# Performance work log

Measured on AMD Instinct MI355X. Metric: run time of the kernel, lower is better.

The kernel has to match this reference:

```python
import jax, jax.numpy as jnp
import numpy as np

B, DIM, Hs, Ws = 2, 64, 48, 48
HEADS, DIM_HEAD = 4, 16
INNER = HEADS * DIM_HEAD  # 64
MLP_DIM = 256


def setup_inputs() -> dict:
    key = jax.random.key(0)
    ks = jax.random.split(key, 10)
    w = lambda k, shape: (jax.random.normal(k, shape, jnp.float32) * 0.02)
    return dict(
        x=jax.random.normal(ks[0], (B, DIM, Hs, Ws), jnp.float32),
        y=jax.random.normal(ks[1], (B, DIM, Hs, Ws), jnp.float32),
        ln1_g=jnp.ones((DIM,), jnp.float32), ln1_b=jnp.zeros((DIM,), jnp.float32),
        w_sa1=w(ks[2], (DIM, INNER)), w_sa2=w(ks[3], (DIM, INNER)),
        w_se1=w(ks[4], (DIM, INNER)), w_se2=w(ks[5], (DIM, INNER)),
        w_out=w(ks[6], (INNER, DIM)), b_out=jnp.zeros((DIM,), jnp.float32),
        ln2_g=jnp.ones((DIM,), jnp.float32), ln2_b=jnp.zeros((DIM,), jnp.float32),
        w1=w(ks[7], (DIM, MLP_DIM)), b1=jnp.zeros((MLP_DIM,), jnp.float32),
        w2=w(ks[8], (MLP_DIM, DIM)), b2=jnp.zeros((DIM,), jnp.float32),
    )


def _layer_norm(t, g, b, eps=1e-5):
    m = t.mean(-1, keepdims=True)
    v = t.var(-1, keepdims=True)
    return (t - m) * jax.lax.rsqrt(v + eps) * g + b


def reference(x, y, ln1_g, ln1_b, w_sa1, w_sa2, w_se1, w_se2, w_out, b_out,
              ln2_g, ln2_b, w1, b1, w2, b2):
    b, c, h, wdt = x.shape
    xt = x.reshape(b, c, h * wdt).transpose(0, 2, 1)  # B n C
    yt = y.reshape(b, c, h * wdt).transpose(0, 2, 1)
    n = xt.shape[1]
    scale = DIM_HEAD ** (-0.5)

    # PreNorm: same LayerNorm applied to both x and y (shared params)
    xn = _layer_norm(xt, ln1_g, ln1_b)
    yn = _layer_norm(yt, ln1_g, ln1_b)

    def split_heads(t, wm):  # B n C -> B h n d
        return (t @ wm).reshape(b, n, HEADS, DIM_HEAD).transpose(0, 2, 1, 3)

    y1 = split_heads(yn, w_sa1)
    y2 = split_heads(yn, w_sa2)
    x1 = split_heads(xn, w_se1)
    x2 = split_heads(xn, w_se2)

    # spatial attention map: n x n from y branch
    sacm = jax.nn.softmax(jnp.einsum('bhid,bhjd->bhij', y1, y2) * scale, axis=-1)
    # channel attention map: d x d from x branch
    secm = jax.nn.softmax(jnp.einsum('bhni,bhnj->bhij', x1, x2) * scale / (n / DIM_HEAD), axis=-1)

    out1 = jnp.einsum('bhij,bhjd->bhid', sacm, x1)  # spatial map applied to x values
    out2 = jnp.einsum('bhni,bhij->bhnj', y1, secm)  # channel map applied to y values
    out = (out1 * out2).transpose(0, 2, 1, 3).reshape(b, n, INNER)
    xt = xt + out @ w_out + b_out  # residual around attention

    # MLP with PreNorm + residual, LeakyReLU slope 0.01 (torch default)
    xn2 = _layer_norm(xt, ln2_g, ln2_b)
    hid = jax.nn.leaky_relu(xn2 @ w1 + b1, negative_slope=0.01)
    xt = xt + hid @ w2 + b2

    return xt.transpose(0, 2, 1).reshape(b, c, h, wdt)
```

## Files before the change

### kernel.cpp

```cpp
#include <hip/hip_runtime.h>

#define HW 2304
#define CH 64
typedef unsigned short ushort_t;
typedef __attribute__((ext_vector_type(8))) short bf16x8;
typedef __attribute__((ext_vector_type(4))) float f32x4;

#define QSCL (0.25f * 1.44269504088896340736f)
#define SECM_SCL (0.25f / 144.f)
#define MFMA(a, b, c) __builtin_amdgcn_mfma_f32_16x16x32_bf16((a), (b), (c), 0, 0, 0)

static __device__ __forceinline__ ushort_t f2bf(float f) {
    union { float f; unsigned u; } v; v.f = f;
    unsigned r = v.u + 0x7FFFu + ((v.u >> 16) & 1u);
    return (ushort_t)(r >> 16);
}
static __device__ __forceinline__ unsigned cvtpk(float a, float b) {
    unsigned r;
    asm("v_cvt_pk_bf16_f32 %0, %1, %2" : "=v"(r) : "v"(a), "v"(b));
    return r;
}
union U8 { unsigned u[4]; bf16x8 v; };

__global__ __launch_bounds__(256) void k_wconv(
    const float* __restrict__ wsa1, const float* __restrict__ wsa2,
    const float* __restrict__ wse1, const float* __restrict__ wse2,
    const float* __restrict__ w_out, const float* __restrict__ w1,
    const float* __restrict__ w2,
    ushort_t* __restrict__ wsa1T, ushort_t* __restrict__ wsa2T,
    ushort_t* __restrict__ wse1T, ushort_t* __restrict__ wse2T,
    ushort_t* __restrict__ w_outT, ushort_t* __restrict__ wT1, ushort_t* __restrict__ wT2,
    float* __restrict__ sacc)
{
    const int blk = blockIdx.x, tid = threadIdx.x;
    if (blk < 8) sacc[blk * 256 + tid] = 0.f;
    if (blk < 80) {
        const int mi = blk >> 4;
        const float* s = mi == 0 ? wsa1 : mi == 1 ? wsa2 : mi == 2 ? wse1 : mi == 3 ? wse2 : w_out;
        ushort_t* d = mi == 0 ? wsa1T : mi == 1 ? wsa2T : mi == 2 ? wse1T : mi == 3 ? wse2T : w_outT;
        const int o = (blk & 15) * 256 + tid;
        d[o] = f2bf(s[(o & 63) * 64 + (o >> 6)]);
    } else if (blk < 144) {
        const int o = (blk - 80) * 256 + tid;
        wT1[o] = f2bf(w1[(o & 63) * 256 + (o >> 6)]);
    } else {
        const int o = (blk - 144) * 256 + tid;
        wT2[o] = f2bf(w2[(o & 255) * 64 + (o >> 8)]);
    }
}

__global__ __launch_bounds__(64) void k_ln_proj(
    const float* __restrict__ x, const float* __restrict__ y,
    const float* __restrict__ g, const float* __restrict__ bb,
    const ushort_t* __restrict__ wsa1T, const ushort_t* __restrict__ wsa2T,
    const ushort_t* __restrict__ wse1T, const ushort_t* __restrict__ wse2T,
    float* __restrict__ y1f, ushort_t* __restrict__ qbf, ushort_t* __restrict__ kbf,
    ushort_t* __restrict__ vtbf, float* __restrict__ sacc)
{
    __shared__ ushort_t ldsA[16 * 24 + 32];
    __shared__ ushort_t ldsB[16 * 24 + 32];
    const int task = blockIdx.x;
    const int jt = blockIdx.y;
    const int rt = task % 144;
    const int b  = (task / 144) & 1;
    const int branch = task / 288;
    const int lane = threadIdx.x;
    const int r = lane & 15, cg = lane >> 4;
    const int q0 = rt * 16;
    const float* in = (branch ? y : x) + (size_t)b * CH * HW + q0 + r;
    float lo[8], hi[8];
    float s = 0.f, sq = 0.f;
    #pragma unroll
    for (int ki = 0; ki < 8; ++ki) {
        lo[ki] = in[(size_t)(8 * cg + ki) * HW];
        hi[ki] = in[(size_t)(32 + 8 * cg + ki) * HW];
        s += lo[ki] + hi[ki];
        sq += lo[ki] * lo[ki] + hi[ki] * hi[ki];
    }
    s  += __shfl_xor(s, 16);  s  += __shfl_xor(s, 32);
    sq += __shfl_xor(sq, 16); sq += __shfl_xor(sq, 32);
    const float m  = s * (1.f / 64.f);
    const float rs = rsqrtf(sq * (1.f / 64.f) - m * m + 1e-5f);
    float ga[16], be[16];
    {
        const float4* gp = (const float4*)g;
        const float4* bp = (const float4*)bb;
        *(float4*)&ga[0]  = gp[2 * cg];     *(float4*)&ga[4]  = gp[2 * cg + 1];
        *(float4*)&ga[8]  = gp[8 + 2 * cg]; *(float4*)&ga[12] = gp[9 + 2 * cg];
        *(float4*)&be[0]  = bp[2 * cg];     *(float4*)&be[4]  = bp[2 * cg + 1];
        *(float4*)&be[8]  = bp[8 + 2 * cg]; *(float4*)&be[12] = bp[9 + 2 * cg];
    }
    float nlo[8], nhi[8];
    #pragma unroll
    for (int ki = 0; ki < 8; ++ki) {
        nlo[ki] = (lo[ki] - m) * rs * ga[ki]     + be[ki];
        nhi[ki] = (hi[ki] - m) * rs * ga[8 + ki] + be[8 + ki];
    }
    U8 alo, ahi;
    #pragma unroll
    for (int p = 0; p < 4; ++p) {
        alo.u[p] = cvtpk(nlo[2 * p], nlo[2 * p + 1]);
        ahi.u[p] = cvtpk(nhi[2 * p], nhi[2 * p + 1]);
    }
    const ushort_t* wp1 = branch ? wsa1T : wse1T;
    const ushort_t* wp2 = branch ? wsa2T : wse2T;
    const f32x4 zero4 = {0.f, 0.f, 0.f, 0.f};
    const int bh = b * 4 + jt;
    bf16x8 bl1 = *(const bf16x8*)(wp1 + (jt * 16 + r) * 64 + 8 * cg);
    bf16x8 bh1 = *(const bf16x8*)(wp1 + (jt * 16 + r) * 64 + 32 + 8 * cg);
    f32x4 acc1 = zero4;
    acc1 = MFMA(alo.v, bl1, acc1);
    acc1 = MFMA(ahi.v, bh1, acc1);
    bf16x8 bl2 = *(const bf16x8*)(wp2 + (jt * 16 + r) * 64 + 8 * cg);
    bf16x8 bh2 = *(const bf16x8*)(wp2 + (jt * 16 + r) * 64 + 32 + 8 * cg);
    f32x4 acc2 = zero4;
    acc2 = MFMA(alo.v, bl2, acc2);
    acc2 = MFMA(ahi.v, bh2, acc2);
    if (branch == 0) {
        uint2 pk1; pk1.x = cvtpk(acc1[0], acc1[1]); pk1.y = cvtpk(acc1[2], acc1[3]);
        *(uint2*)(vtbf + (size_t)(bh * 16 + r) * HW + q0 + 4 * cg) = pk1;
        *(uint2*)&ldsA[r * 24 + 4 * cg] = pk1;
        uint2 pk2; pk2.x = cvtpk(acc2[0], acc2[1]); pk2.y = cvtpk(acc2[2], acc2[3]);
        *(uint2*)&ldsB[r * 24 + 4 * cg] = pk2;
        bf16x8 af = {0, 0, 0, 0, 0, 0, 0, 0};
        bf16x8 bf_ = {0, 0, 0, 0, 0, 0, 0, 0};
        if (cg < 2) {
            af  = *(const bf16x8*)&ldsA[r * 24 + 8 * cg];
            bf_ = *(const bf16x8*)&ldsB[r * 24 + 8 * cg];
        }
        f32x4 sp = MFMA(af, bf_, zero4);
        #pragma unroll
        for (int ri = 0; ri < 4; ++ri)
            atomicAdd(&sacc[bh * 256 + (4 * cg + ri) * 16 + r], sp[ri]);
    } else {
        #pragma unroll
        for (int ri = 0; ri < 4; ++ri) {
            const int q = q0 + 4 * cg + ri;
            y1f[((size_t)bh * HW + q) * 16 + r] = acc1[ri];
            qbf[((size_t)bh * HW + q) * 16 + r] = f2bf(acc1[ri] * QSCL);
            kbf[((size_t)bh * HW + q) * 16 + r] = f2bf(acc2[ri]);
        }
    }
}

__global__ __launch_bounds__(512) void k_attn(
    const ushort_t* __restrict__ qbf, const ushort_t* __restrict__ kbf,
    const ushort_t* __restrict__ vtbf, const float* __restrict__ y1f,
    const float* __restrict__ sacc, ushort_t* __restrict__ obf)
{
    __shared__ uint4 pbuf4[8][80];
    __shared__ f32x4 cacc[8][64];
    __shared__ float clsum[8][64];
    __shared__ float sraw[256];
    __shared__ float smv[256];
    const int qt = blockIdx.x, bh = blockIdx.y;
    const int tid = threadIdx.x;
    const int w = tid >> 6, lane = tid & 63;
    const int q16 = lane & 15, g = lane >> 4;
    const int q0 = qt * 16;
    if (tid < 256) sraw[tid] = sacc[bh * 256 + tid] * SECM_SCL;
    __syncthreads();
    if (tid < 256) {
        const int i = tid >> 4;
        float mx = -1e30f;
        #pragma unroll
        for (int jj = 0; jj < 16; ++jj) mx = fmaxf(mx, sraw[i * 16 + jj]);
        float sum = 0.f;
        #pragma unroll
        for (int jj = 0; jj < 16; ++jj) sum += __expf(sraw[i * 16 + jj] - mx);
        smv[tid] = __expf(sraw[tid] - mx) / sum;
    }

    bf16x8 qfrag = {0, 0, 0, 0, 0, 0, 0, 0};
    if (g < 2) qfrag = *(const bf16x8*)(qbf + ((size_t)bh * HW + q0 + q16) * 16 + g * 8);

    unsigned char* pw = (unsigned char*)&pbuf4[w][0];
    const ushort_t* kbase = kbf + (size_t)bh * HW * 16;
    const ushort_t* vbase = vtbf + (size_t)(bh * 16 + q16) * HW;
    f32x4 oacc = {0.f, 0.f, 0.f, 0.f};
    float lsum = 0.f;
    const f32x4 zero4 = {0.f, 0.f, 0.f, 0.f};

    #pragma unroll 3
    for (int wi = 0; wi < 9; ++wi) {
        const int k0 = w * 288 + wi * 32;
        bf16x8 kf0 = *(const bf16x8*)(kbase + (size_t)(k0 + q16) * 16 + (g & 1) * 8);
        bf16x8 kf1 = *(const bf16x8*)(kbase + (size_t)(k0 + 16 + q16) * 16 + (g & 1) * 8);
        f32x4 s0 = MFMA(kf0, qfrag, zero4);
        f32x4 s1 = MFMA(kf1, qfrag, zero4);
        const float e00 = exp2f(s0[0]), e01 = exp2f(s0[1]), e02 = exp2f(s0[2]), e03 = exp2f(s0[3]);
        const float e10 = exp2f(s1[0]), e11 = exp2f(s1[1]), e12 = exp2f(s1[2]), e13 = exp2f(s1[3]);
        lsum += ((e00 + e01) + (e02 + e03)) + ((e10 + e11) + (e12 + e13));
        *(unsigned*)(pw + q16 * 80 + 8 * g)      = cvtpk(e00, e01);
        *(unsigned*)(pw + q16 * 80 + 8 * g + 4)  = cvtpk(e02, e03);
        *(unsigned*)(pw + q16 * 80 + 32 + 8 * g) = cvtpk(e10, e11);
        *(unsigned*)(pw + q16 * 80 + 36 + 8 * g) = cvtpk(e12, e13);
        bf16x8 vfrag = *(const bf16x8*)(vbase + k0 + 8 * g);
        bf16x8 pfrag = *(const bf16x8*)(pw + q16 * 80 + 16 * g);
        oacc = MFMA(vfrag, pfrag, oacc);
    }
    cacc[w][lane] = oacc;
    clsum[w][lane] = lsum;
    __syncthreads();
    if (tid < 64) {
        f32x4 t = cacc[0][lane];
        float L = clsum[0][lane];
        #pragma unroll
        for (int ww = 1; ww < 8; ++ww) {
            f32x4 tw = cacc[ww][lane];
            t[0] += tw[0]; t[1] += tw[1]; t[2] += tw[2]; t[3] += tw[3];
            L += clsum[ww][lane];
        }
        L += __shfl_xor(L, 16);
        L += __shfl_xor(L, 32);
        const float invl = 1.f / L;
        const float* yrow = y1f + ((size_t)bh * HW + q0 + q16) * 16;
        float ya[16];
        #pragma unroll
        for (int i = 0; i < 4; ++i) *(float4*)&ya[4 * i] = ((const float4*)yrow)[i];
        float gate[4] = {0.f, 0.f, 0.f, 0.f};
        #pragma unroll
        for (int i = 0; i < 16; ++i) {
            #pragma unroll
            for (int rr = 0; rr < 4; ++rr) gate[rr] += ya[i] * smv[i * 16 + g * 4 + rr];
        }
        const int b = bh >> 2, h = bh & 3;
        float r0 = t[0] * invl * gate[0];
        float r1 = t[1] * invl * gate[1];
        float r2 = t[2] * invl * gate[2];
        float r3 = t[3] * invl * gate[3];
        uint2 pk; pk.x = cvtpk(r0, r1); pk.y = cvtpk(r2, r3);
        *(uint2*)(obf + ((size_t)b * HW + q0 + q16) * 64 + h * 16 + g * 4) = pk;
    }
}

__global__ __launch_bounds__(256) void k_tail(
    const ushort_t* __restrict__ obf, const float* __restrict__ x,
    const ushort_t* __restrict__ w_outT, const float* __restrict__ b_out,
    const float* __restrict__ g2, const float* __restrict__ bt2,
    const ushort_t* __restrict__ wT1, const float* __restrict__ b1,
    const ushort_t* __restrict__ wT2, const float* __restrict__ b2,
    float* __restrict__ out)
{
    __shared__ float xtile[16][68];
    __shared__ ushort_t hh[16 * 264 + 16];
    const int t = blockIdx.x;
    const int b = t / 144;
    const int q0 = (t % 144) * 16;
    const int tid = threadIdx.x;
    const int w = tid >> 6, lane = tid & 63;
    const int r = lane & 15, cg = lane >> 4;
    const f32x4 zero4 = {0.f, 0.f, 0.f, 0.f};
    const ushort_t* arow = obf + ((size_t)b * HW + q0 + r) * 64;
    bf16x8 alo = *(const bf16x8*)(arow + 8 * cg);
    bf16x8 ahi = *(const bf16x8*)(arow + 32 + 8 * cg);
    {
        bf16x8 bl = *(const bf16x8*)(w_outT + (w * 16 + r) * 64 + 8 * cg);
        bf16x8 bh_ = *(const bf16x8*)(w_outT + (w * 16 + r) * 64 + 32 + 8 * cg);
        f32x4 acc = zero4;
        acc = MFMA(alo, bl, acc);
        acc = MFMA(ahi, bh_, acc);
        const int c = w * 16 + r;
        const float bo = b_out[c];
        float4 xr = *(const float4*)(x + (size_t)b * CH * HW + (size_t)c * HW + q0 + 4 * cg);
        xtile[4 * cg + 0][c] = acc[0] + bo + xr.x;
        xtile[4 * cg + 1][c] = acc[1] + bo + xr.y;
        xtile[4 * cg + 2][c] = acc[2] + bo + xr.z;
        xtile[4 * cg + 3][c] = acc[3] + bo + xr.w;
    }
    __syncthreads();
    float s = 0.f, sq = 0.f;
    #pragma unroll
    for (int j = 0; j < 16; ++j) {
        const float v = xtile[r][cg * 16 + j];
        s += v; sq += v * v;
    }
    s  += __shfl_xor(s, 16);  s  += __shfl_xor(s, 32);
    sq += __shfl_xor(sq, 16); sq += __shfl_xor(sq, 32);
    const float m  = s * (1.f / 64.f);
    const float rs = rsqrtf(sq * (1.f / 64.f) - m * m + 1e-5f);
    float ga[16], be[16];
    {
        const float4* gp = (const float4*)g2;
        const float4* bp = (const float4*)bt2;
        *(float4*)&ga[0]  = gp[2 * cg];     *(float4*)&ga[4]  = gp[2 * cg + 1];
        *(float4*)&ga[8]  = gp[8 + 2 * cg]; *(float4*)&ga[12] = gp[9 + 2 * cg];
        *(float4*)&be[0]  = bp[2 * cg];     *(float4*)&be[4]  = bp[2 * cg + 1];
        *(float4*)&be[8]  = bp[8 + 2 * cg]; *(float4*)&be[12] = bp[9 + 2 * cg];
    }
    float nlo[8], nhi[8];
    #pragma unroll
    for (int ki = 0; ki < 8; ++ki) {
        nlo[ki] = (xtile[r][8 * cg + ki]      - m) * rs * ga[ki]     + be[ki];
        nhi[ki] = (xtile[r][32 + 8 * cg + ki] - m) * rs * ga[8 + ki] + be[8 + ki];
    }
    U8 axlo, axhi;
    #pragma unroll
    for (int p = 0; p < 4; ++p) {
        axlo.u[p] = cvtpk(nlo[2 * p], nlo[2 * p + 1]);
        axhi.u[p] = cvtpk(nhi[2 * p], nhi[2 * p + 1]);
    }
    #pragma unroll
    for (int jj = 0; jj < 4; ++jj) {
        const int jt = 4 * w + jj;
        bf16x8 bl = *(const bf16x8*)(wT1 + (jt * 16 + r) * 64 + 8 * cg);
        bf16x8 bh_ = *(const bf16x8*)(wT1 + (jt * 16 + r) * 64 + 32 + 8 * cg);
        f32x4 acc = zero4;
        acc = MFMA(axlo.v, bl, acc);
        acc = MFMA(axhi.v, bh_, acc);
        const int c = jt * 16 + r;
        const float bias = b1[c];
        #pragma unroll
        for (int ri = 0; ri < 4; ++ri) {
            float vv = acc[ri] + bias;
            vv = fmaxf(vv, 0.01f * vv);
            hh[(4 * cg + ri) * 264 + c] = f2bf(vv);
        }
    }
    __syncthreads();
    bf16x8 ha[8];
    #pragma unroll
    for (int kw = 0; kw < 8; ++kw)
        ha[kw] = *(const bf16x8*)&hh[r * 264 + kw * 32 + 8 * cg];
    f32x4 acc = zero4;
    #pragma unroll
    for (int kw = 0; kw < 8; ++kw) {
        bf16x8 bf_ = *(const bf16x8*)(wT2 + (w * 16 + r) * 256 + kw * 32 + 8 * cg);
        acc = MFMA(ha[kw], bf_, acc);
    }
    const int c = w * 16 + r;
    const float bias = b2[c];
    float4 res;
    res.x = acc[0] + bias + xtile[4 * cg + 0][c];
    res.y = acc[1] + bias + xtile[4 * cg + 1][c];
    res.z = acc[2] + bias + xtile[4 * cg + 2][c];
    res.w = acc[3] + bias + xtile[4 * cg + 3][c];
    *(float4*)(out + (size_t)b * CH * HW + (size_t)c * HW + q0 + 4 * cg) = res;
}

extern "C" void kernel_launch(void* const* d_in, const int* in_sizes, int n_in,
                              void* d_out, int out_size, void* d_ws, size_t ws_size,
                              hipStream_t stream)
{
    (void)in_sizes; (void)n_in; (void)out_size; (void)ws_size;
    const float* x     = (const float*)d_in[0];
    const float* y     = (const float*)d_in[1];
    const float* ln1_g = (const float*)d_in[2];
    const float* ln1_b = (const float*)d_in[3];
    const float* w_sa1 = (const float*)d_in[4];
    const float* w_sa2 = (const float*)d_in[5];
    const float* w_se1 = (const float*)d_in[6];
    const float* w_se2 = (const float*)d_in[7];
    const float* w_out = (const float*)d_in[8];
    const float* b_out = (const float*)d_in[9];
    const float* ln2_g = (const float*)d_in[10];
    const float* ln2_b = (const float*)d_in[11];
    const float* w1    = (const float*)d_in[12];
    const float* b1    = (const float*)d_in[13];
    const float* w2    = (const float*)d_in[14];
    const float* b2    = (const float*)d_in[15];
    float* out = (float*)d_out;

    const size_t NP = 8ull * HW * 16;
    float* p = (float*)d_ws;
    float* y1f  = p;  p += NP;
    float* sacc = p;  p += 2048;
    ushort_t* u = (ushort_t*)p;
    ushort_t* qbf   = u;  u += NP;
    ushort_t* kbf   = u;  u += NP;
    ushort_t* vtbf  = u;  u += NP;
    ushort_t* obf   = u;  u += NP;
    ushort_t* wsa1T = u;  u += 4096;
    ushort_t* wsa2T = u;  u += 4096;
    ushort_t* wse1T = u;  u += 4096;
    ushort_t* wse2T = u;  u += 4096;
    ushort_t* w_outT= u;  u += 4096;
    ushort_t* wT1   = u;  u += 16384;
    ushort_t* wT2   = u;  u += 16384;

    k_wconv<<<208, 256, 0, stream>>>(w_sa1, w_sa2, w_se1, w_se2, w_out, w1, w2,
                                     wsa1T, wsa2T, wse1T, wse2T, w_outT, wT1, wT2,
                                     sacc);
    k_ln_proj<<<dim3(576, 4), 64, 0, stream>>>(x, y, ln1_g, ln1_b,
                                               wsa1T, wsa2T, wse1T, wse2T,
                                               y1f, qbf, kbf, vtbf, sacc);
    k_attn<<<dim3(144, 8), 512, 0, stream>>>(qbf, kbf, vtbf, y1f, sacc, obf);
    k_tail<<<288, 256, 0, stream>>>(obf, x, w_outT, b_out, ln2_g, ln2_b,
                                    wT1, b1, wT2, b2, out);
}
```

Before: 119.3 us.

## Drop weight-conversion kernel and atomics; recompute channel map inside attention blocks

```diff
diff --git a/kernel.cpp b/kernel.cpp
--- a/kernel.cpp
+++ b/kernel.cpp
@@ -7,6 +7,7 @@
 typedef __attribute__((ext_vector_type(4))) float f32x4;
 
 #define QSCL (0.25f * 1.44269504088896340736f)
+#define INV_QSCL (1.0f / QSCL)
 #define SECM_SCL (0.25f / 144.f)
 #define MFMA(a, b, c) __builtin_amdgcn_mfma_f32_16x16x32_bf16((a), (b), (c), 0, 0, 0)
 
@@ -15,6 +16,10 @@
     unsigned r = v.u + 0x7FFFu + ((v.u >> 16) & 1u);
     return (ushort_t)(r >> 16);
 }
+static __device__ __forceinline__ float bf2f(ushort_t b) {
+    union { unsigned u; float f; } v; v.u = ((unsigned)b) << 16;
+    return v.f;
+}
 static __device__ __forceinline__ unsigned cvtpk(float a, float b) {
     unsigned r;
     asm("v_cvt_pk_bf16_f32 %0, %1, %2" : "=v"(r) : "v"(a), "v"(b));
@@ -22,43 +27,14 @@
 }
 union U8 { unsigned u[4]; bf16x8 v; };
 
-__global__ __launch_bounds__(256) void k_wconv(
-    const float* __restrict__ wsa1, const float* __restrict__ wsa2,
-    const float* __restrict__ wse1, const float* __restrict__ wse2,
-    const float* __restrict__ w_out, const float* __restrict__ w1,
-    const float* __restrict__ w2,
-    ushort_t* __restrict__ wsa1T, ushort_t* __restrict__ wsa2T,
-    ushort_t* __restrict__ wse1T, ushort_t* __restrict__ wse2T,
-    ushort_t* __restrict__ w_outT, ushort_t* __restrict__ wT1, ushort_t* __restrict__ wT2,
-    float* __restrict__ sacc)
-{
-    const int blk = blockIdx.x, tid = threadIdx.x;
-    if (blk < 8) sacc[blk * 256 + tid] = 0.f;
-    if (blk < 80) {
-        const int mi = blk >> 4;
-        const float* s = mi == 0 ? wsa1 : mi == 1 ? wsa2 : mi == 2 ? wse1 : mi == 3 ? wse2 : w_out;
-        ushort_t* d = mi == 0 ? wsa1T : mi == 1 ? wsa2T : mi == 2 ? wse1T : mi == 3 ? wse2T : w_outT;
-        const int o = (blk & 15) * 256 + tid;
-        d[o] = f2bf(s[(o & 63) * 64 + (o >> 6)]);
-    } else if (blk < 144) {
-        const int o = (blk - 80) * 256 + tid;
-        wT1[o] = f2bf(w1[(o & 63) * 256 + (o >> 6)]);
-    } else {
-        const int o = (blk - 144) * 256 + tid;
-        wT2[o] = f2bf(w2[(o & 255) * 64 + (o >> 8)]);
-    }
-}
-
 __global__ __launch_bounds__(64) void k_ln_proj(
     const float* __restrict__ x, const float* __restrict__ y,
     const float* __restrict__ g, const float* __restrict__ bb,
-    const ushort_t* __restrict__ wsa1T, const ushort_t* __restrict__ wsa2T,
-    const ushort_t* __restrict__ wse1T, const ushort_t* __restrict__ wse2T,
-    float* __restrict__ y1f, ushort_t* __restrict__ qbf, ushort_t* __restrict__ kbf,
-    ushort_t* __restrict__ vtbf, float* __restrict__ sacc)
+    const float* __restrict__ wsa1, const float* __restrict__ wsa2,
+    const float* __restrict__ wse1, const float* __restrict__ wse2,
+    ushort_t* __restrict__ qbf, ushort_t* __restrict__ kbf,
+    ushort_t* __restrict__ vtbf, ushort_t* __restrict__ x2t)
 {
-    __shared__ ushort_t ldsA[16 * 24 + 32];
-    __shared__ ushort_t ldsB[16 * 24 + 32];
     const int task = blockIdx.x;
     const int jt = blockIdx.y;
     const int rt = task % 144;
@@ -67,6 +43,17 @@
     const int lane = threadIdx.x;
     const int r = lane & 15, cg = lane >> 4;
     const int q0 = rt * 16;
+    const float* wp1 = branch ? wsa1 : wse1;
+    const float* wp2 = branch ? wsa2 : wse2;
+    const int oc = jt * 16 + r;
+    U8 bl1, bh1, bl2, bh2;
+    #pragma unroll
+    for (int p = 0; p < 4; ++p) {
+        bl1.u[p] = cvtpk(wp1[(8 * cg + 2 * p) * 64 + oc],      wp1[(8 * cg + 2 * p + 1) * 64 + oc]);
+        bh1.u[p] = cvtpk(wp1[(32 + 8 * cg + 2 * p) * 64 + oc], wp1[(32 + 8 * cg + 2 * p + 1) * 64 + oc]);
+        bl2.u[p] = cvtpk(wp2[(8 * cg + 2 * p) * 64 + oc],      wp2[(8 * cg + 2 * p + 1) * 64 + oc]);
+        bh2.u[p] = cvtpk(wp2[(32 + 8 * cg + 2 * p) * 64 + oc], wp2[(32 + 8 * cg + 2 * p + 1) * 64 + oc]);
+    }
     const float* in = (branch ? y : x) + (size_t)b * CH * HW + q0 + r;
     float lo[8], hi[8];
     float s = 0.f, sq = 0.f;
@@ -102,41 +89,23 @@
         alo.u[p] = cvtpk(nlo[2 * p], nlo[2 * p + 1]);
         ahi.u[p] = cvtpk(nhi[2 * p], nhi[2 * p + 1]);
     }
-    const ushort_t* wp1 = branch ? wsa1T : wse1T;
-    const ushort_t* wp2 = branch ? wsa2T : wse2T;
     const f32x4 zero4 = {0.f, 0.f, 0.f, 0.f};
     const int bh = b * 4 + jt;
-    bf16x8 bl1 = *(const bf16x8*)(wp1 + (jt * 16 + r) * 64 + 8 * cg);
-    bf16x8 bh1 = *(const bf16x8*)(wp1 + (jt * 16 + r) * 64 + 32 + 8 * cg);
     f32x4 acc1 = zero4;
-    acc1 = MFMA(alo.v, bl1, acc1);
-    acc1 = MFMA(ahi.v, bh1, acc1);
-    bf16x8 bl2 = *(const bf16x8*)(wp2 + (jt * 16 + r) * 64 + 8 * cg);
-    bf16x8 bh2 = *(const bf16x8*)(wp2 + (jt * 16 + r) * 64 + 32 + 8 * cg);
+    acc1 = MFMA(alo.v, bl1.v, acc1);
+    acc1 = MFMA(ahi.v, bh1.v, acc1);
     f32x4 acc2 = zero4;
-    acc2 = MFMA(alo.v, bl2, acc2);
-    acc2 = MFMA(ahi.v, bh2, acc2);
+    acc2 = MFMA(alo.v, bl2.v, acc2);
+    acc2 = MFMA(ahi.v, bh2.v, acc2);
     if (branch == 0) {
         uint2 pk1; pk1.x = cvtpk(acc1[0], acc1[1]); pk1.y = cvtpk(acc1[2], acc1[3]);
         *(uint2*)(vtbf + (size_t)(bh * 16 + r) * HW + q0 + 4 * cg) = pk1;
-        *(uint2*)&ldsA[r * 24 + 4 * cg] = pk1;
         uint2 pk2; pk2.x = cvtpk(acc2[0], acc2[1]); pk2.y = cvtpk(acc2[2], acc2[3]);
-        *(uint2*)&ldsB[r * 24 + 4 * cg] = pk2;
-        bf16x8 af = {0, 0, 0, 0, 0, 0, 0, 0};
-        bf16x8 bf_ = {0, 0, 0, 0, 0, 0, 0, 0};
-        if (cg < 2) {
-            af  = *(const bf16x8*)&ldsA[r * 24 + 8 * cg];
-            bf_ = *(const bf16x8*)&ldsB[r * 24 + 8 * cg];
-        }
-        f32x4 sp = MFMA(af, bf_, zero4);
-        #pragma unroll
-        for (int ri = 0; ri < 4; ++ri)
-            atomicAdd(&sacc[bh * 256 + (4 * cg + ri) * 16 + r], sp[ri]);
+        *(uint2*)(x2t + (size_t)(bh * 16 + r) * HW + q0 + 4 * cg) = pk2;
     } else {
         #pragma unroll
         for (int ri = 0; ri < 4; ++ri) {
             const int q = q0 + 4 * cg + ri;
-            y1f[((size_t)bh * HW + q) * 16 + r] = acc1[ri];
             qbf[((size_t)bh * HW + q) * 16 + r] = f2bf(acc1[ri] * QSCL);
             kbf[((size_t)bh * HW + q) * 16 + r] = f2bf(acc2[ri]);
         }
@@ -145,31 +114,19 @@
 
 __global__ __launch_bounds__(512) void k_attn(
     const ushort_t* __restrict__ qbf, const ushort_t* __restrict__ kbf,
-    const ushort_t* __restrict__ vtbf, const float* __restrict__ y1f,
-    const float* __restrict__ sacc, ushort_t* __restrict__ obf)
+    const ushort_t* __restrict__ vtbf, const ushort_t* __restrict__ x2t,
+    ushort_t* __restrict__ obf)
 {
     __shared__ uint4 pbuf4[8][80];
     __shared__ f32x4 cacc[8][64];
     __shared__ float clsum[8][64];
-    __shared__ float sraw[256];
+    __shared__ f32x4 csec[8][64];
     __shared__ float smv[256];
     const int qt = blockIdx.x, bh = blockIdx.y;
     const int tid = threadIdx.x;
     const int w = tid >> 6, lane = tid & 63;
     const int q16 = lane & 15, g = lane >> 4;
     const int q0 = qt * 16;
-    if (tid < 256) sraw[tid] = sacc[bh * 256 + tid] * SECM_SCL;
-    __syncthreads();
-    if (tid < 256) {
-        const int i = tid >> 4;
-        float mx = -1e30f;
-        #pragma unroll
-        for (int jj = 0; jj < 16; ++jj) mx = fmaxf(mx, sraw[i * 16 + jj]);
-        float sum = 0.f;
-        #pragma unroll
-        for (int jj = 0; jj < 16; ++jj) sum += __expf(sraw[i * 16 + jj] - mx);
-        smv[tid] = __expf(sraw[tid] - mx) / sum;
-    }
 
     bf16x8 qfrag = {0, 0, 0, 0, 0, 0, 0, 0};
     if (g < 2) qfrag = *(const bf16x8*)(qbf + ((size_t)bh * HW + q0 + q16) * 16 + g * 8);
@@ -177,7 +134,9 @@
     unsigned char* pw = (unsigned char*)&pbuf4[w][0];
     const ushort_t* kbase = kbf + (size_t)bh * HW * 16;
     const ushort_t* vbase = vtbf + (size_t)(bh * 16 + q16) * HW;
+    const ushort_t* x2base = x2t + (size_t)(bh * 16 + q16) * HW;
     f32x4 oacc = {0.f, 0.f, 0.f, 0.f};
+    f32x4 scacc = {0.f, 0.f, 0.f, 0.f};
     float lsum = 0.f;
     const f32x4 zero4 = {0.f, 0.f, 0.f, 0.f};
 
@@ -186,8 +145,11 @@
         const int k0 = w * 288 + wi * 32;
         bf16x8 kf0 = *(const bf16x8*)(kbase + (size_t)(k0 + q16) * 16 + (g & 1) * 8);
         bf16x8 kf1 = *(const bf16x8*)(kbase + (size_t)(k0 + 16 + q16) * 16 + (g & 1) * 8);
+        bf16x8 vfrag = *(const bf16x8*)(vbase + k0 + 8 * g);
+        bf16x8 x2frag = *(const bf16x8*)(x2base + k0 + 8 * g);
         f32x4 s0 = MFMA(kf0, qfrag, zero4);
         f32x4 s1 = MFMA(kf1, qfrag, zero4);
+        scacc = MFMA(vfrag, x2frag, scacc);
         const float e00 = exp2f(s0[0]), e01 = exp2f(s0[1]), e02 = exp2f(s0[2]), e03 = exp2f(s0[3]);
         const float e10 = exp2f(s1[0]), e11 = exp2f(s1[1]), e12 = exp2f(s1[2]), e13 = exp2f(s1[3]);
         lsum += ((e00 + e01) + (e02 + e03)) + ((e10 + e11) + (e12 + e13));
@@ -195,29 +157,44 @@
         *(unsigned*)(pw + q16 * 80 + 8 * g + 4)  = cvtpk(e02, e03);
         *(unsigned*)(pw + q16 * 80 + 32 + 8 * g) = cvtpk(e10, e11);
         *(unsigned*)(pw + q16 * 80 + 36 + 8 * g) = cvtpk(e12, e13);
-        bf16x8 vfrag = *(const bf16x8*)(vbase + k0 + 8 * g);
         bf16x8 pfrag = *(const bf16x8*)(pw + q16 * 80 + 16 * g);
         oacc = MFMA(vfrag, pfrag, oacc);
     }
     cacc[w][lane] = oacc;
     clsum[w][lane] = lsum;
+    csec[w][lane] = scacc;
     __syncthreads();
     if (tid < 64) {
-        f32x4 t = cacc[0][lane];
+        f32x4 tt = cacc[0][lane];
+        f32x4 sc = csec[0][lane];
         float L = clsum[0][lane];
         #pragma unroll
         for (int ww = 1; ww < 8; ++ww) {
             f32x4 tw = cacc[ww][lane];
-            t[0] += tw[0]; t[1] += tw[1]; t[2] += tw[2]; t[3] += tw[3];
+            f32x4 sw = csec[ww][lane];
+            tt[0] += tw[0]; tt[1] += tw[1]; tt[2] += tw[2]; tt[3] += tw[3];
+            sc[0] += sw[0]; sc[1] += sw[1]; sc[2] += sw[2]; sc[3] += sw[3];
             L += clsum[ww][lane];
         }
         L += __shfl_xor(L, 16);
         L += __shfl_xor(L, 32);
         const float invl = 1.f / L;
-        const float* yrow = y1f + ((size_t)bh * HW + q0 + q16) * 16;
+        #pragma unroll
+        for (int ri = 0; ri < 4; ++ri) {
+            float v = sc[ri] * SECM_SCL;
+            float mx = v;
+            mx = fmaxf(mx, __shfl_xor(mx, 1)); mx = fmaxf(mx, __shfl_xor(mx, 2));
+            mx = fmaxf(mx, __shfl_xor(mx, 4)); mx = fmaxf(mx, __shfl_xor(mx, 8));
+            const float e = __expf(v - mx);
+            float su = e;
+            su += __shfl_xor(su, 1); su += __shfl_xor(su, 2);
+            su += __shfl_xor(su, 4); su += __shfl_xor(su, 8);
+            smv[(4 * g + ri) * 16 + q16] = e / su;
+        }
+        const ushort_t* yrow = qbf + ((size_t)bh * HW + q0 + q16) * 16;
         float ya[16];
         #pragma unroll
-        for (int i = 0; i < 4; ++i) *(float4*)&ya[4 * i] = ((const float4*)yrow)[i];
+        for (int i = 0; i < 16; ++i) ya[i] = bf2f(yrow[i]) * INV_QSCL;
         float gate[4] = {0.f, 0.f, 0.f, 0.f};
         #pragma unroll
         for (int i = 0; i < 16; ++i) {
@@ -225,10 +202,10 @@
             for (int rr = 0; rr < 4; ++rr) gate[rr] += ya[i] * smv[i * 16 + g * 4 + rr];
         }
         const int b = bh >> 2, h = bh & 3;
-        float r0 = t[0] * invl * gate[0];
-        float r1 = t[1] * invl * gate[1];
-        float r2 = t[2] * invl * gate[2];
-        float r3 = t[3] * invl * gate[3];
+        float r0 = tt[0] * invl * gate[0];
+        float r1 = tt[1] * invl * gate[1];
+        float r2 = tt[2] * invl * gate[2];
+        float r3 = tt[3] * invl * gate[3];
         uint2 pk; pk.x = cvtpk(r0, r1); pk.y = cvtpk(r2, r3);
         *(uint2*)(obf + ((size_t)b * HW + q0 + q16) * 64 + h * 16 + g * 4) = pk;
     }
@@ -236,10 +213,10 @@
 
 __global__ __launch_bounds__(256) void k_tail(
     const ushort_t* __restrict__ obf, const float* __restrict__ x,
-    const ushort_t* __restrict__ w_outT, const float* __restrict__ b_out,
+    const float* __restrict__ w_out, const float* __restrict__ b_out,
     const float* __restrict__ g2, const float* __restrict__ bt2,
-    const ushort_t* __restrict__ wT1, const float* __restrict__ b1,
-    const ushort_t* __restrict__ wT2, const float* __restrict__ b2,
+    const float* __restrict__ w1, const float* __restrict__ mb1,
+    const float* __restrict__ w2, const float* __restrict__ mb2,
     float* __restrict__ out)
 {
     __shared__ float xtile[16][68];
@@ -255,18 +232,22 @@
     bf16x8 alo = *(const bf16x8*)(arow + 8 * cg);
     bf16x8 ahi = *(const bf16x8*)(arow + 32 + 8 * cg);
     {
-        bf16x8 bl = *(const bf16x8*)(w_outT + (w * 16 + r) * 64 + 8 * cg);
-        bf16x8 bh_ = *(const bf16x8*)(w_outT + (w * 16 + r) * 64 + 32 + 8 * cg);
+        const int oc = w * 16 + r;
+        U8 bl, bh_;
+        #pragma unroll
+        for (int p = 0; p < 4; ++p) {
+            bl.u[p]  = cvtpk(w_out[(8 * cg + 2 * p) * 64 + oc],      w_out[(8 * cg + 2 * p + 1) * 64 + oc]);
+            bh_.u[p] = cvtpk(w_out[(32 + 8 * cg + 2 * p) * 64 + oc], w_out[(32 + 8 * cg + 2 * p + 1) * 64 + oc]);
+        }
         f32x4 acc = zero4;
-        acc = MFMA(alo, bl, acc);
-        acc = MFMA(ahi, bh_, acc);
-        const int c = w * 16 + r;
-        const float bo = b_out[c];
-        float4 xr = *(const float4*)(x + (size_t)b * CH * HW + (size_t)c * HW + q0 + 4 * cg);
-        xtile[4 * cg + 0][c] = acc[0] + bo + xr.x;
-        xtile[4 * cg + 1][c] = acc[1] + bo + xr.y;
-        xtile[4 * cg + 2][c] = acc[2] + bo + xr.z;
-        xtile[4 * cg + 3][c] = acc[3] + bo + xr.w;
+        acc = MFMA(alo, bl.v, acc);
+        acc = MFMA(ahi, bh_.v, acc);
+        const float bo = b_out[oc];
+        float4 xr = *(const float4*)(x + (size_t)b * CH * HW + (size_t)oc * HW + q0 + 4 * cg);
+        xtile[4 * cg + 0][oc] = acc[0] + bo + xr.x;
+        xtile[4 * cg + 1][oc] = acc[1] + bo + xr.y;
+        xtile[4 * cg + 2][oc] = acc[2] + bo + xr.z;
+        xtile[4 * cg + 3][oc] = acc[3] + bo + xr.w;
     }
     __syncthreads();
     float s = 0.f, sq = 0.f;
@@ -303,39 +284,44 @@
     #pragma unroll
     for (int jj = 0; jj < 4; ++jj) {
         const int jt = 4 * w + jj;
-        bf16x8 bl = *(const bf16x8*)(wT1 + (jt * 16 + r) * 64 + 8 * cg);
-        bf16x8 bh_ = *(const bf16x8*)(wT1 + (jt * 16 + r) * 64 + 32 + 8 * cg);
+        const int hc = jt * 16 + r;
+        U8 bl, bh_;
+        #pragma unroll
+        for (int p = 0; p < 4; ++p) {
+            bl.u[p]  = cvtpk(w1[(8 * cg + 2 * p) * 256 + hc],      w1[(8 * cg + 2 * p + 1) * 256 + hc]);
+            bh_.u[p] = cvtpk(w1[(32 + 8 * cg + 2 * p) * 256 + hc], w1[(32 + 8 * cg + 2 * p + 1) * 256 + hc]);
+        }
         f32x4 acc = zero4;
-        acc = MFMA(axlo.v, bl, acc);
-        acc = MFMA(axhi.v, bh_, acc);
-        const int c = jt * 16 + r;
-        const float bias = b1[c];
+        acc = MFMA(axlo.v, bl.v, acc);
+        acc = MFMA(axhi.v, bh_.v, acc);
+        const float bias = mb1[hc];
         #pragma unroll
         for (int ri = 0; ri < 4; ++ri) {
             float vv = acc[ri] + bias;
             vv = fmaxf(vv, 0.01f * vv);
-            hh[(4 * cg + ri) * 264 + c] = f2bf(vv);
+            hh[(4 * cg + ri) * 264 + hc] = f2bf(vv);
         }
     }
     __syncthreads();
-    bf16x8 ha[8];
-    #pragma unroll
-    for (int kw = 0; kw < 8; ++kw)
-        ha[kw] = *(const bf16x8*)&hh[r * 264 + kw * 32 + 8 * cg];
+    const int oc = w * 16 + r;
     f32x4 acc = zero4;
     #pragma unroll
     for (int kw = 0; kw < 8; ++kw) {
-        bf16x8 bf_ = *(const bf16x8*)(wT2 + (w * 16 + r) * 256 + kw * 32 + 8 * cg);
-        acc = MFMA(ha[kw], bf_, acc);
-    }
-    const int c = w * 16 + r;
-    const float bias = b2[c];
+        bf16x8 ha = *(const bf16x8*)&hh[r * 264 + kw * 32 + 8 * cg];
+        U8 bf_;
+        #pragma unroll
+        for (int p = 0; p < 4; ++p)
+            bf_.u[p] = cvtpk(w2[(kw * 32 + 8 * cg + 2 * p) * 64 + oc],
+                             w2[(kw * 32 + 8 * cg + 2 * p + 1) * 64 + oc]);
+        acc = MFMA(ha, bf_.v, acc);
+    }
+    const float bias = mb2[oc];
     float4 res;
-    res.x = acc[0] + bias + xtile[4 * cg + 0][c];
-    res.y = acc[1] + bias + xtile[4 * cg + 1][c];
-    res.z = acc[2] + bias + xtile[4 * cg + 2][c];
-    res.w = acc[3] + bias + xtile[4 * cg + 3][c];
-    *(float4*)(out + (size_t)b * CH * HW + (size_t)c * HW + q0 + 4 * cg) = res;
+    res.x = acc[0] + bias + xtile[4 * cg + 0][oc];
+    res.y = acc[1] + bias + xtile[4 * cg + 1][oc];
+    res.z = acc[2] + bias + xtile[4 * cg + 2][oc];
+    res.w = acc[3] + bias + xtile[4 * cg + 3][oc];
+    *(float4*)(out + (size_t)b * CH * HW + (size_t)oc * HW + q0 + 4 * cg) = res;
 }
 
 extern "C" void kernel_launch(void* const* d_in, const int* in_sizes, int n_in,
@@ -362,29 +348,17 @@
     float* out = (float*)d_out;
 
     const size_t NP = 8ull * HW * 16;
-    float* p = (float*)d_ws;
-    float* y1f  = p;  p += NP;
-    float* sacc = p;  p += 2048;
-    ushort_t* u = (ushort_t*)p;
+    ushort_t* u = (ushort_t*)d_ws;
     ushort_t* qbf   = u;  u += NP;
     ushort_t* kbf   = u;  u += NP;
     ushort_t* vtbf  = u;  u += NP;
+    ushort_t* x2t   = u;  u += NP;
     ushort_t* obf   = u;  u += NP;
-    ushort_t* wsa1T = u;  u += 4096;
-    ushort_t* wsa2T = u;  u += 4096;
-    ushort_t* wse1T = u;  u += 4096;
-    ushort_t* wse2T = u;  u += 4096;
-    ushort_t* w_outT= u;  u += 4096;
-    ushort_t* wT1   = u;  u += 16384;
-    ushort_t* wT2   = u;  u += 16384;
-
-    k_wconv<<<208, 256, 0, stream>>>(w_sa1, w_sa2, w_se1, w_se2, w_out, w1, w2,
-                                     wsa1T, wsa2T, wse1T, wse2T, w_outT, wT1, wT2,
-                                     sacc);
+
     k_ln_proj<<<dim3(576, 4), 64, 0, stream>>>(x, y, ln1_g, ln1_b,
-                                               wsa1T, wsa2T, wse1T, wse2T,
-                                               y1f, qbf, kbf, vtbf, sacc);
-    k_attn<<<dim3(144, 8), 512, 0, stream>>>(qbf, kbf, vtbf, y1f, sacc, obf);
-    k_tail<<<288, 256, 0, stream>>>(obf, x, w_outT, b_out, ln2_g, ln2_b,
-                                    wT1, b1, wT2, b2, out);
-}
+                                               w_sa1, w_sa2, w_se1, w_se2,
+                                               qbf, kbf, vtbf, x2t);
+    k_attn<<<dim3(144, 8), 512, 0, stream>>>(qbf, kbf, vtbf, x2t, obf);
+    k_tail<<<288, 256, 0, stream>>>(obf, x, w_out, b_out, ln2_g, ln2_b,
+                                    w1, b1, w2, b2, out);
+}
```

Measured after the change: 124.8 us. 4.6% more time.
